# Kernel tuning notes

Measured on AMD Instinct MI355X. Metric: run time of the kernel, lower is better.

The kernel has to match this reference:

```python
import jax, jax.numpy as jnp
import numpy as np

B, A, GS = 4, 256, 12           # graphs, atoms per graph, grid size
NG = GS ** 3                    # 1728 grid nodes per graph
K_A, K_G = 8, 32                # atom kNN, grid->atom kNN
L, CODE, HID, EDGE = 4, 64, 128, 64
NTYPES, NGAUSS, CUT, SPACING = 16, 20, 5.0, 1.5
N_NODES = B * A + B * NG


def _grid_coords():
    half = (GS - 1) * SPACING / 2.0
    g = jnp.linspace(-half, half, GS)
    mesh = jnp.meshgrid(g, g, g, indexing='ij')
    return jnp.stack(mesh, axis=-1).reshape(-1, 3)  # [NG, 3]


def _gauss_consts():
    # GaussianSmearing(type_='exp', start=0, stop=cutoff, num_gaussians=20)
    off = jnp.exp(jnp.linspace(np.log(1.0), np.log(CUT + 1.0), NGAUSS)) - 1.0
    d = jnp.diff(off)
    d = jnp.concatenate([d[:1], d])
    return off, -0.5 / d ** 2


def _build_edges(pos):
    # pos: [B*A, 3] atom coords, per-graph kNN (batch = 256 atoms per graph)
    atom_pos = pos.reshape(B, A, 3)
    # atom-atom kNN (loop=False): edge (neighbor j -> atom i)
    d2 = jnp.sum((atom_pos[:, :, None, :] - atom_pos[:, None, :, :]) ** 2, -1)
    d2 = d2 + jnp.eye(A) * 1e9  # exclude self loops
    _, nbr = jax.lax.top_k(-d2, K_A)                       # [B, A, K_A]
    src_a = (nbr + (jnp.arange(B) * A)[:, None, None]).reshape(-1)
    dst_a = jnp.repeat(jnp.arange(B * A), K_A)
    # grid->atom kNN: each grid node receives from its K_G nearest atoms
    grid = _grid_coords()
    gd2 = jnp.sum((grid[None, :, None, :] - atom_pos[:, None, :, :]) ** 2, -1)  # [B, NG, A]
    _, gn = jax.lax.top_k(-gd2, K_G)                       # [B, NG, K_G]
    src_g = (gn + (jnp.arange(B) * A)[:, None, None]).reshape(-1)
    dst_g = B * A + jnp.repeat(jnp.arange(B * NG), K_G)
    return jnp.concatenate([src_a, src_g]), jnp.concatenate([dst_a, dst_g])


def _layer(h, node_pos, src, dst, cnt, off, coeff, eW, eb, W1, b1, W2, b2, g, beta):
    rel = node_pos[src] - node_pos[dst]
    dist = jnp.clip(jnp.sqrt(jnp.sum(rel ** 2, -1)), 0.0, CUT)
    gauss = jnp.exp(coeff * (dist[:, None] - off) ** 2)    # [E, 20]
    ef = gauss @ eW + eb                                   # [E, EDGE]
    mi = jnp.concatenate([h[src], h[dst], ef], -1)         # [E, 2*CODE+EDGE]
    m = jax.nn.relu(mi @ W1 + b1) @ W2 + b2                # [E, CODE]
    aggr = jax.ops.segment_sum(m, dst, num_segments=N_NODES) / cnt[:, None]
    x = h + aggr
    mu = jnp.mean(x, -1, keepdims=True)
    var = jnp.var(x, -1, keepdims=True)
    return (x - mu) / jnp.sqrt(var + 1e-5) * g + beta


def setup_inputs() -> dict:
    key = jax.random.key(0)
    ks = jax.random.split(key, 6)
    s = 0.05
    return {
        'pos': jax.random.uniform(ks[0], (B * A, 3), minval=-8.0, maxval=8.0),
        'atom_types': jax.random.randint(ks[1], (B * A,), 0, NTYPES),
        'batch': jnp.repeat(jnp.arange(B), A),
        'edge_W': jax.random.normal(ks[2], (L, NGAUSS, EDGE)) * s,
        'edge_b': jnp.zeros((L, EDGE)),
        'W1': jax.random.normal(ks[3], (L, 2 * CODE + EDGE, HID)) * s,
        'b1': jnp.zeros((L, HID)),
        'W2': jax.random.normal(ks[4], (L, HID, CODE)) * s,
        'b2': jnp.zeros((L, CODE)),
        'ln_g': jnp.ones((L, CODE)),
        'ln_b': jnp.zeros((L, CODE)),
    }


def reference(pos, atom_types, batch, edge_W, edge_b, W1, b1, W2, b2, ln_g, ln_b):
    # node features: one-hot atoms padded to code_dim, zero grid codes
    af = jax.nn.one_hot(atom_types, NTYPES, dtype=jnp.float32)
    af = jnp.pad(af, ((0, 0), (0, CODE - NTYPES)))
    h = jnp.concatenate([af, jnp.zeros((B * NG, CODE), jnp.float32)], 0)
    node_pos = jnp.concatenate([pos, jnp.tile(_grid_coords(), (B, 1))], 0)
    src, dst = _build_edges(pos)
    cnt = jnp.clip(jax.ops.segment_sum(jnp.ones_like(dst, jnp.float32), dst,
                                       num_segments=N_NODES), 1.0)
    off, coeff = _gauss_consts()
    for l in range(L):
        h = _layer(h, node_pos, src, dst, cnt, off, coeff,
                   edge_W[l], edge_b[l], W1[l], b1[l], W2[l], b2[l],
                   ln_g[l], ln_b[l])
    return h[B * A:].reshape(B, NG, CODE)
```

## Files before the change

kernel.cpp:

```cpp
#include <hip/hip_runtime.h>
#include <hip/hip_bf16.h>
#include <math.h>

#define NATOMS 1024
#define NGRID  6912
#define NNODES 7936
#define NG_PER 1728
#define KA 8
#define KG 32
#define CODE 64
#define HID 128
#define NT 1024

typedef __hip_bfloat16 bf16;
typedef unsigned long long u64;
typedef unsigned int u32;

static void* g_buf = nullptr;
__attribute__((constructor)) static void _alloc_ws(){
  if (hipMalloc(&g_buf, (size_t)24 * 1024 * 1024) != hipSuccess) g_buf = nullptr;
}

__device__ __forceinline__ float ldf(const void* p, size_t i, int f32){
  return f32 ? ((const float*)p)[i] : __bfloat162float(((const bf16*)p)[i]);
}

__device__ __forceinline__ int ldt(const void* p, int i, int mode){
  switch(mode){
    case 1:  return ((const int*)p)[2*i];
    case 2:  return (int)((const float*)p)[i];
    case 3:  return (int)__bfloat162float(((const bf16*)p)[i]);
    default: return ((const int*)p)[i];
  }
}

__global__ void k0(const unsigned short* __restrict__ posu,
                   const unsigned short* __restrict__ typu,
                   int* __restrict__ flag, float* __restrict__ offc){
  if (blockIdx.x == 0){
    __shared__ int scnt;
    int t = threadIdx.x;
    if (t == 0) scnt = 0;
    __syncthreads();
    int c = 0;
    for (int q = 0; q < 12; q++){
      unsigned short u = posu[t + 256*q];
      int e = (u >> 7) & 0xFF;
      if (e >= 140) c++;
    }
    atomicAdd(&scnt, c);
    __syncthreads();
    if (t == 0) flag[0] = (scnt > 16) ? 1 : 0;
  } else {
    if (threadIdx.x == 0){
      int oddHigh = 0, evenHigh = 0, quadZero = 1;
      for (int k = 0; k < 16; k++){
        unsigned short o = typu[2*k+1], e = typu[2*k];
        if (o >= 0x3F00 && o <= 0x4200) oddHigh++;
        if (e >= 0x3F00 && e <= 0x4200) evenHigh++;
      }
      for (int k = 0; k < 16; k++) if (typu[4*k+2] != 0) quadZero = 0;
      int mode;
      if (oddHigh >= 8) mode = (evenHigh >= 8) ? 3 : 2;
      else              mode = quadZero ? 1 : 0;
      flag[1] = mode;
    }
    int k = (int)threadIdx.x - 64;
    if (k >= 0 && k < 20){
      double step = log(6.0) / 19.0;
      double offk = exp((double)k * step) - 1.0;
      int km = (k == 0) ? 1 : k;
      double d = (exp((double)km * step) - 1.0) - (exp((double)(km - 1) * step) - 1.0);
      offc[k]      = (float)offk;
      offc[20 + k] = (float)(-0.5 / (d * d));
    }
  }
}

__global__ void __launch_bounds__(256) k_pre(const void* __restrict__ pos,
    const void* __restrict__ types, const int* __restrict__ flag,
    float* __restrict__ node_pos, float* __restrict__ h0,
    int* __restrict__ nbrA, int* __restrict__ nbrG){
  #pragma clang fp contract(off)
  int f32 = flag[0];
  int b = blockIdx.x;
  int t = threadIdx.x;
  if (b < 1984){
    int tm = flag[1];
    int idx = b * 256 + t;
    if (idx < NNODES){
      if (idx < NATOMS){
        node_pos[idx*3+0] = ldf(pos, idx*3+0, f32);
        node_pos[idx*3+1] = ldf(pos, idx*3+1, f32);
        node_pos[idx*3+2] = ldf(pos, idx*3+2, f32);
      } else {
        int cell = (idx - NATOMS) % NG_PER;
        int ix = cell / 144, iy = (cell / 12) % 12, iz = cell % 12;
        node_pos[idx*3+0] = -8.25f + 1.5f * ix;
        node_pos[idx*3+1] = -8.25f + 1.5f * iy;
        node_pos[idx*3+2] = -8.25f + 1.5f * iz;
      }
    }
    int node = idx >> 6, c = idx & 63;
    float v = 0.f;
    if (node < NATOMS && c == ldt(types, node, tm)) v = 1.f;
    h0[idx] = v;
  } else if (b < 1984 + 256){
    int i = (b - 1984) * 4 + (t >> 6);
    int bb = i >> 8, li = i & 255;
    int l = t & 63;
    float px = ldf(pos,3*i,f32), py = ldf(pos,3*i+1,f32), pz = ldf(pos,3*i+2,f32);
    u64 vals[4];
    for (int q = 0; q < 4; q++){
      int c = l + 64*q;
      int j = (bb << 8) + c;
      float dx = ldf(pos,3*j+0,f32) - px;
      float dy = ldf(pos,3*j+1,f32) - py;
      float dz = ldf(pos,3*j+2,f32) - pz;
      float d2 = (dx*dx + dy*dy) + dz*dz;
      vals[q] = (c == li) ? ~0ull : (((u64)__float_as_uint(d2) << 8) | (unsigned)c);
    }
    for (int it = 0; it < KA; it++){
      u64 v = vals[0];
      for (int q = 1; q < 4; q++) if (vals[q] < v) v = vals[q];
      for (int m = 1; m < 64; m <<= 1){
        u64 ov = __shfl_xor(v, m);
        if (ov < v) v = ov;
      }
      int widx = (int)(v & 0xFF);
      if (l == 0) nbrA[i*KA + it] = (bb << 8) + widx;
      if ((widx & 63) == l) vals[widx >> 6] = ~0ull;
    }
  } else {
    int gi = (b - 2240) * 4 + (t >> 6);
    int bb = gi / NG_PER, cell = gi % NG_PER;
    int ix = cell / 144, iy = (cell / 12) % 12, iz = cell % 12;
    double px = -8.25 + 1.5 * ix;
    double py = -8.25 + 1.5 * iy;
    double pz = -8.25 + 1.5 * iz;
    int l = t & 63;
    u64 vals[4];
    for (int q = 0; q < 4; q++){
      int c = l + 64*q;
      int j = (bb << 8) + c;
      double dx = px - (double)ldf(pos,3*j+0,f32);
      double dy = py - (double)ldf(pos,3*j+1,f32);
      double dz = pz - (double)ldf(pos,3*j+2,f32);
      double d2 = dx*dx + dy*dy + dz*dz;
      vals[q] = ((u64)__double_as_longlong(d2) & ~0xFFull) | (unsigned)c;
    }
    for (int it = 0; it < KG; it++){
      u64 v = vals[0];
      for (int q = 1; q < 4; q++) if (vals[q] < v) v = vals[q];
      for (int m = 1; m < 64; m <<= 1){
        u64 ov = __shfl_xor(v, m);
        if (ov < v) v = ov;
      }
      int widx = (int)(v & 0xFF);
      if (l == 0) nbrG[gi*KG + it] = (bb << 8) + widx;
      if ((widx & 63) == l) vals[widx >> 6] = ~0ull;
    }
  }
}

__global__ void __launch_bounds__(128) k_fold(const float* __restrict__ hin,
    const void* __restrict__ W1, const void* __restrict__ b1,
    const void* __restrict__ eW, const void* __restrict__ eb,
    size_t wl, size_t b1o, size_t eWo, size_t ebo,
    const int* __restrict__ flag,
    float* __restrict__ Xd, float* __restrict__ Xs,
    float* __restrict__ Wg, float* __restrict__ b1p,
    const float* __restrict__ offc, float* __restrict__ Tt)
{
  __shared__ __attribute__((aligned(16))) float sA[1344];
  __shared__ float sB[160];
  int f32 = flag[0];
  int t = threadIdx.x;
  int b = blockIdx.x;
  if (b < 1120){
    int isXd = (b < 992);
    size_t wo = wl + (isXd ? (size_t)64*128 : 0);
    int r0 = (isXd ? b : (b - 992)) * 8;
    float* C = isXd ? Xd : Xs;
    float w[64];
    #pragma unroll
    for (int k = 0; k < 64; k++) w[k] = ldf(W1, wo + (size_t)k*128 + t, f32);
    for (int i = t; i < 8*64; i += 128) sA[i] = hin[(size_t)r0*64 + i];
    __syncthreads();
    #pragma unroll
    for (int r = 0; r < 8; r += 4){
      float a0 = 0.f, a1 = 0.f, a2 = 0.f, a3 = 0.f;
      #pragma unroll
      for (int k4 = 0; k4 < 16; k4++){
        float4 v0 = *(const float4*)&sA[(r+0)*64 + 4*k4];
        float4 v1 = *(const float4*)&sA[(r+1)*64 + 4*k4];
        float4 v2 = *(const float4*)&sA[(r+2)*64 + 4*k4];
        float4 v3 = *(const float4*)&sA[(r+3)*64 + 4*k4];
        a0 = fmaf(v0.x, w[4*k4+0], a0); a0 = fmaf(v0.y, w[4*k4+1], a0);
        a0 = fmaf(v0.z, w[4*k4+2], a0); a0 = fmaf(v0.w, w[4*k4+3], a0);
        a1 = fmaf(v1.x, w[4*k4+0], a1); a1 = fmaf(v1.y, w[4*k4+1], a1);
        a1 = fmaf(v1.z, w[4*k4+2], a1); a1 = fmaf(v1.w, w[4*k4+3], a1);
        a2 = fmaf(v2.x, w[4*k4+0], a2); a2 = fmaf(v2.y, w[4*k4+1], a2);
        a2 = fmaf(v2.z, w[4*k4+2], a2); a2 = fmaf(v2.w, w[4*k4+3], a2);
        a3 = fmaf(v3.x, w[4*k4+0], a3); a3 = fmaf(v3.y, w[4*k4+1], a3);
        a3 = fmaf(v3.z, w[4*k4+2], a3); a3 = fmaf(v3.w, w[4*k4+3], a3);
      }
      C[(size_t)(r0 + r + 0)*128 + t] = a0;
      C[(size_t)(r0 + r + 1)*128 + t] = a1;
      C[(size_t)(r0 + r + 2)*128 + t] = a2;
      C[(size_t)(r0 + r + 3)*128 + t] = a3;
    }
  } else if (b == 1120){
    float w[64];
    #pragma unroll
    for (int k = 0; k < 64; k++) w[k] = ldf(W1, wl + (size_t)128*128 + (size_t)k*128 + t, f32);
    for (int i = t; i < 20*64; i += 128) sA[i] = ldf(eW, eWo + i, f32);
    if (t < 64) sA[1280 + t] = ldf(eb, ebo + t, f32);
    __syncthreads();
    for (int g = 0; g < 20; g++){
      float acc = 0.f;
      #pragma unroll
      for (int k4 = 0; k4 < 16; k4++){
        float4 e = *(const float4*)&sA[g*64 + 4*k4];
        acc = fmaf(e.x, w[4*k4+0], acc); acc = fmaf(e.y, w[4*k4+1], acc);
        acc = fmaf(e.z, w[4*k4+2], acc); acc = fmaf(e.w, w[4*k4+3], acc);
      }
      Wg[g*128 + t] = acc;
    }
    float acc = ldf(b1, b1o + t, f32);
    #pragma unroll
    for (int k4 = 0; k4 < 16; k4++){
      float4 e = *(const float4*)&sA[1280 + 4*k4];
      acc = fmaf(e.x, w[4*k4+0], acc); acc = fmaf(e.y, w[4*k4+1], acc);
      acc = fmaf(e.z, w[4*k4+2], acc); acc = fmaf(e.w, w[4*k4+3], acc);
    }
    b1p[t] = acc;
  } else {
    int r0 = (b - 1121) * 8;
    float w[64];
    #pragma unroll
    for (int k = 0; k < 64; k++) w[k] = ldf(W1, wl + (size_t)128*128 + (size_t)k*128 + t, f32);
    for (int i = t; i < 20*64; i += 128) sA[i] = ldf(eW, eWo + i, f32);
    for (int i = t; i < 160; i += 128){
      int row = i / 20, k = i - row*20;
      float d  = (float)(r0 + row) * (5.0f / (float)NT);
      float dd = d - offc[k];
      sB[i] = expf(offc[20 + k] * dd * dd);
    }
    __syncthreads();
    float wg[20];
    #pragma unroll
    for (int gk = 0; gk < 20; gk++){
      float acc = 0.f;
      #pragma unroll
      for (int k4 = 0; k4 < 16; k4++){
        float4 e = *(const float4*)&sA[gk*64 + 4*k4];
        acc = fmaf(e.x, w[4*k4+0], acc); acc = fmaf(e.y, w[4*k4+1], acc);
        acc = fmaf(e.z, w[4*k4+2], acc); acc = fmaf(e.w, w[4*k4+3], acc);
      }
      wg[gk] = acc;
    }
    #pragma unroll
    for (int r = 0; r < 8; r++){
      int row = r0 + r;
      if (row <= NT){
        float acc = 0.f;
        #pragma unroll
        for (int k = 0; k < 20; k++) acc = fmaf(sB[r*20 + k], wg[k], acc);
        Tt[(size_t)row*128 + t] = acc;
      }
    }
  }
}

__global__ void __launch_bounds__(256) k_aggr(const float* __restrict__ Xs,
    const float* __restrict__ Xd, const int* __restrict__ nbrA,
    const int* __restrict__ nbrG, const float* __restrict__ node_pos,
    const float* __restrict__ Tt, const float* __restrict__ b1p,
    float* __restrict__ Sbuf)
{
  __shared__ __attribute__((aligned(16))) int   sN[256];
  __shared__ __attribute__((aligned(16))) float sX[256];
  int t = threadIdx.x;
  int b = blockIdx.x;
  int KK, node0; const int* nbr;
  if (b < 32){ KK = 8;  node0 = b*32;              nbr = nbrA + b*256; }
  else       { KK = 32; node0 = NATOMS + (b-32)*8; nbr = nbrG + (size_t)(b-32)*256; }
  {
    int src = nbr[t];
    sN[t] = src;
    int node = node0 + ((b < 32) ? (t >> 3) : (t >> 5));
    float dx = node_pos[src*3+0] - node_pos[node*3+0];
    float dy = node_pos[src*3+1] - node_pos[node*3+1];
    float dz = node_pos[src*3+2] - node_pos[node*3+2];
    float dist = fminf(sqrtf(dx*dx + dy*dy + dz*dz), 5.0f);
    sX[t] = dist * ((float)NT / 5.0f);
  }
  int g = t >> 7, tt = t & 127;
  float b1v = b1p[tt];
  __syncthreads();
  float rK = 1.f / KK;
  int nLoc = (b < 32) ? 16 : 4;
  int nbase = g * nLoc;
  for (int n = 0; n < nLoc; n++){
    int node = node0 + nbase + n;
    float zb = Xd[(size_t)node*128 + tt] + b1v;
    float S = 0.f;
    int ebase = (nbase + n) * KK;
    for (int e = 0; e < KK; e += 4){
      int i0 = ebase + e;
      int4   sv = *(const int4*)&sN[i0];
      float4 xv = *(const float4*)&sX[i0];
      int ia0 = (int)xv.x; if (ia0 > NT-1) ia0 = NT-1;
      int ia1 = (int)xv.y; if (ia1 > NT-1) ia1 = NT-1;
      int ia2 = (int)xv.z; if (ia2 > NT-1) ia2 = NT-1;
      int ia3 = (int)xv.w; if (ia3 > NT-1) ia3 = NT-1;
      float f0 = xv.x - (float)ia0;
      float f1 = xv.y - (float)ia1;
      float f2 = xv.z - (float)ia2;
      float f3 = xv.w - (float)ia3;
      const float* t0 = Tt + (size_t)ia0*128 + tt;
      const float* t1 = Tt + (size_t)ia1*128 + tt;
      const float* t2 = Tt + (size_t)ia2*128 + tt;
      const float* t3 = Tt + (size_t)ia3*128 + tt;
      float v00 = t0[0], v01 = t0[128];
      float v10 = t1[0], v11 = t1[128];
      float v20 = t2[0], v21 = t2[128];
      float v30 = t3[0], v31 = t3[128];
      float a0 = zb + Xs[(size_t)sv.x*128 + tt] + fmaf(f0, v01 - v00, v00);
      float a1 = zb + Xs[(size_t)sv.y*128 + tt] + fmaf(f1, v11 - v10, v10);
      float a2 = zb + Xs[(size_t)sv.z*128 + tt] + fmaf(f2, v21 - v20, v20);
      float a3 = zb + Xs[(size_t)sv.w*128 + tt] + fmaf(f3, v31 - v30, v30);
      S += fmaxf(a0,0.f) + fmaxf(a1,0.f) + fmaxf(a2,0.f) + fmaxf(a3,0.f);
    }
    Sbuf[(size_t)node*128 + tt] = S * rK;
  }
}

__global__ void __launch_bounds__(256) k_out(const float* __restrict__ hin,
    const float* __restrict__ Sbuf,
    const void* __restrict__ W2, const void* __restrict__ b2,
    const void* __restrict__ lng, const void* __restrict__ lnb,
    size_t w2o, size_t b2o, size_t lno,
    const int* __restrict__ flag,
    float* __restrict__ hout, float* __restrict__ out, int writeOut)
{
  __shared__ float sW2[128*64];
  __shared__ __attribute__((aligned(16))) float sS[32*128];
  int f32 = flag[0];
  int t = threadIdx.x;
  int r0 = blockIdx.x * 32;
  for (int i = t; i < 128*64; i += 256) sW2[i] = ldf(W2, w2o + i, f32);
  for (int i = t; i < 32*128; i += 256) sS[i] = Sbuf[(size_t)r0*128 + i];
  int w = t >> 6, c = t & 63;
  float b2v = ldf(b2, b2o + c, f32);
  float gv  = ldf(lng, lno + c, f32);
  float bv  = ldf(lnb, lno + c, f32);
  __syncthreads();
  for (int rr = w*8; rr < w*8 + 8; rr += 2){
    float a0 = 0.f, a1 = 0.f;
    const float* s0 = &sS[rr*128];
    const float* s1 = &sS[(rr+1)*128];
    #pragma unroll
    for (int kq = 0; kq < 32; kq++){
      float4 sv0 = *(const float4*)(s0 + 4*kq);
      float4 sv1 = *(const float4*)(s1 + 4*kq);
      a0 = fmaf(sv0.x, sW2[(4*kq+0)*64+c], a0);
      a0 = fmaf(sv0.y, sW2[(4*kq+1)*64+c], a0);
      a0 = fmaf(sv0.z, sW2[(4*kq+2)*64+c], a0);
      a0 = fmaf(sv0.w, sW2[(4*kq+3)*64+c], a0);
      a1 = fmaf(sv1.x, sW2[(4*kq+0)*64+c], a1);
      a1 = fmaf(sv1.y, sW2[(4*kq+1)*64+c], a1);
      a1 = fmaf(sv1.z, sW2[(4*kq+2)*64+c], a1);
      a1 = fmaf(sv1.w, sW2[(4*kq+3)*64+c], a1);
    }
    {
      int node = r0 + rr;
      float x = hin[(size_t)node*64 + c] + a0 + b2v;
      float s = x;
      #pragma unroll
      for (int m = 1; m < 64; m <<= 1) s += __shfl_xor(s, m);
      float mu = s * (1.f/64.f);
      float d = x - mu;
      float v = d * d;
      #pragma unroll
      for (int m = 1; m < 64; m <<= 1) v += __shfl_xor(v, m);
      v *= (1.f/64.f);
      float o = d / sqrtf(v + 1e-5f) * gv + bv;
      hout[(size_t)node*64 + c] = o;
      if (writeOut && node >= NATOMS) out[(size_t)(node - NATOMS)*64 + c] = o;
    }
    {
      int node = r0 + rr + 1;
      float x = hin[(size_t)node*64 + c] + a1 + b2v;
      float s = x;
      #pragma unroll
      for (int m = 1; m < 64; m <<= 1) s += __shfl_xor(s, m);
      float mu = s * (1.f/64.f);
      float d = x - mu;
      float v = d * d;
      #pragma unroll
      for (int m = 1; m < 64; m <<= 1) v += __shfl_xor(v, m);
      v *= (1.f/64.f);
      float o = d / sqrtf(v + 1e-5f) * gv + bv;
      hout[(size_t)node*64 + c] = o;
      if (writeOut && node >= NATOMS) out[(size_t)(node - NATOMS)*64 + c] = o;
    }
  }
}

extern "C" void kernel_launch(void* const* d_in, const int* in_sizes, int n_in,
                              void* d_out, int out_size, void* d_ws, size_t ws_size,
                              hipStream_t stream) {
  const void* pos    = d_in[0];
  const void* types  = d_in[1];
  const void* edge_W = d_in[3];
  const void* edge_b = d_in[4];
  const void* W1     = d_in[5];
  const void* b1     = d_in[6];
  const void* W2     = d_in[7];
  const void* b2     = d_in[8];
  const void* lng    = d_in[9];
  const void* lnb    = d_in[10];

  const size_t NEED = (size_t)16 * 1024 * 1024;
  char* w = (ws_size >= NEED) ? (char*)d_ws : (char*)g_buf;
  if (w == nullptr) w = (char*)d_ws;

  size_t o = 0;
  auto alloc = [&](size_t bytes)->char*{
    char* r = w + o; o = (o + bytes + 255) & ~(size_t)255; return r;
  };
  float*  node_pos = (float*) alloc((size_t)NNODES*3*4);
  float*  hA       = (float*) alloc((size_t)NNODES*CODE*4);
  float*  hB       = (float*) alloc((size_t)NNODES*CODE*4);
  float*  Xs       = (float*) alloc((size_t)NATOMS*HID*4);
  float*  Xd       = (float*) alloc((size_t)NNODES*HID*4);
  float*  Sbuf     = (float*) alloc((size_t)NNODES*HID*4);
  int*    nbrA     = (int*)   alloc((size_t)NATOMS*KA*4);
  int*    nbrG     = (int*)   alloc((size_t)NGRID*KG*4);
  float*  offc     = (float*) alloc(64*4);
  float*  Wg       = (float*) alloc(20*HID*4);
  float*  b1p      = (float*) alloc(HID*4);
  int*    flag     = (int*)   alloc(64*4);
  float*  Tt       = (float*) alloc((size_t)(NT+1)*HID*4);

  k0<<<2, 256, 0, stream>>>((const unsigned short*)pos,
                            (const unsigned short*)types, flag, offc);
  k_pre<<<3968, 256, 0, stream>>>(pos, types, flag, node_pos, hA, nbrA, nbrG);

  float* hin = hA; float* hout = hB;
  for (int l = 0; l < 4; l++){
    size_t wl  = (size_t)l*192*128;
    size_t eWo = (size_t)l*20*64, ebo = (size_t)l*64;
    size_t b1o = (size_t)l*128,   w2o = (size_t)l*128*64;
    size_t b2o = (size_t)l*64,    lno = (size_t)l*64;
    k_fold<<<1121 + 129, 128, 0, stream>>>(hin, W1, b1, edge_W, edge_b,
                                     wl, b1o, eWo, ebo, flag, Xd, Xs, Wg, b1p,
                                     offc, Tt);
    k_aggr<<<32 + NGRID/8, 256, 0, stream>>>(Xs, Xd, nbrA, nbrG, node_pos,
                                             Tt, b1p, Sbuf);
    k_out<<<NNODES/32, 256, 0, stream>>>(hin, Sbuf, W2, b2, lng, lnb,
                                         w2o, b2o, lno, flag,
                                         hout, (float*)d_out, (l == 3) ? 1 : 0);
    float* tmp = hin; hin = hout; hout = tmp;
  }
}
```

Measured before the change: 359.6 us.

## Replace iterative grid kNN selection with rank counting; pack lerp table pairs

New measurement: 371.8 us. 3.4% more time.

```diff
diff --git a/kernel.cpp b/kernel.cpp
--- a/kernel.cpp
+++ b/kernel.cpp
@@ -82,6 +82,7 @@
     float* __restrict__ node_pos, float* __restrict__ h0,
     int* __restrict__ nbrA, int* __restrict__ nbrG){
   #pragma clang fp contract(off)
+  __shared__ __attribute__((aligned(16))) u64 sK[4][256];
   int f32 = flag[0];
   int b = blockIdx.x;
   int t = threadIdx.x;
@@ -132,14 +133,17 @@
       if ((widx & 63) == l) vals[widx >> 6] = ~0ull;
     }
   } else {
-    int gi = (b - 2240) * 4 + (t >> 6);
+    int w  = t >> 6;
+    int gi = (b - 2240) * 4 + w;
     int bb = gi / NG_PER, cell = gi % NG_PER;
     int ix = cell / 144, iy = (cell / 12) % 12, iz = cell % 12;
     double px = -8.25 + 1.5 * ix;
     double py = -8.25 + 1.5 * iy;
     double pz = -8.25 + 1.5 * iz;
     int l = t & 63;
+    u64* sk = &sK[w][0];
     u64 vals[4];
+    #pragma unroll
     for (int q = 0; q < 4; q++){
       int c = l + 64*q;
       int j = (bb << 8) + c;
@@ -147,19 +151,25 @@
       double dy = py - (double)ldf(pos,3*j+1,f32);
       double dz = pz - (double)ldf(pos,3*j+2,f32);
       double d2 = dx*dx + dy*dy + dz*dz;
-      vals[q] = ((u64)__double_as_longlong(d2) & ~0xFFull) | (unsigned)c;
-    }
-    for (int it = 0; it < KG; it++){
-      u64 v = vals[0];
-      for (int q = 1; q < 4; q++) if (vals[q] < v) v = vals[q];
-      for (int m = 1; m < 64; m <<= 1){
-        u64 ov = __shfl_xor(v, m);
-        if (ov < v) v = ov;
-      }
-      int widx = (int)(v & 0xFF);
-      if (l == 0) nbrG[gi*KG + it] = (bb << 8) + widx;
-      if ((widx & 63) == l) vals[widx >> 6] = ~0ull;
-    }
+      u64 key = ((u64)__double_as_longlong(d2) & ~0xFFull) | (unsigned)c;
+      vals[q] = key;
+      sk[c] = key;
+    }
+    __syncthreads();
+    int r0 = 0, r1 = 0, r2 = 0, r3 = 0;
+    #pragma unroll 4
+    for (int j = 0; j < 256; j += 2){
+      ulonglong2 kk = *(const ulonglong2*)&sk[j];
+      r0 += (kk.x < vals[0]); r0 += (kk.y < vals[0]);
+      r1 += (kk.x < vals[1]); r1 += (kk.y < vals[1]);
+      r2 += (kk.x < vals[2]); r2 += (kk.y < vals[2]);
+      r3 += (kk.x < vals[3]); r3 += (kk.y < vals[3]);
+    }
+    int base = (bb << 8) + l;
+    if (r0 < KG) nbrG[gi*KG + r0] = base;
+    if (r1 < KG) nbrG[gi*KG + r1] = base + 64;
+    if (r2 < KG) nbrG[gi*KG + r2] = base + 128;
+    if (r3 < KG) nbrG[gi*KG + r3] = base + 192;
   }
 }
 
@@ -170,10 +180,10 @@
     const int* __restrict__ flag,
     float* __restrict__ Xd, float* __restrict__ Xs,
     float* __restrict__ Wg, float* __restrict__ b1p,
-    const float* __restrict__ offc, float* __restrict__ Tt)
+    const float* __restrict__ offc, float2* __restrict__ Tt)
 {
   __shared__ __attribute__((aligned(16))) float sA[1344];
-  __shared__ float sB[160];
+  __shared__ float sB[192];
   int f32 = flag[0];
   int t = threadIdx.x;
   int b = blockIdx.x;
@@ -241,7 +251,7 @@
     #pragma unroll
     for (int k = 0; k < 64; k++) w[k] = ldf(W1, wl + (size_t)128*128 + (size_t)k*128 + t, f32);
     for (int i = t; i < 20*64; i += 128) sA[i] = ldf(eW, eWo + i, f32);
-    for (int i = t; i < 160; i += 128){
+    for (int i = t; i < 180; i += 128){
       int row = i / 20, k = i - row*20;
       float d  = (float)(r0 + row) * (5.0f / (float)NT);
       float dd = d - offc[k];
@@ -260,23 +270,24 @@
       }
       wg[gk] = acc;
     }
-    #pragma unroll
-    for (int r = 0; r < 8; r++){
-      int row = r0 + r;
-      if (row <= NT){
-        float acc = 0.f;
-        #pragma unroll
-        for (int k = 0; k < 20; k++) acc = fmaf(sB[r*20 + k], wg[k], acc);
-        Tt[(size_t)row*128 + t] = acc;
-      }
-    }
+    float v[9];
+    #pragma unroll
+    for (int r = 0; r < 9; r++){
+      float acc = 0.f;
+      #pragma unroll
+      for (int k = 0; k < 20; k++) acc = fmaf(sB[r*20 + k], wg[k], acc);
+      v[r] = acc;
+    }
+    #pragma unroll
+    for (int r = 0; r < 8; r++)
+      Tt[(size_t)(r0 + r)*128 + t] = make_float2(v[r], v[r+1]);
   }
 }
 
 __global__ void __launch_bounds__(256) k_aggr(const float* __restrict__ Xs,
     const float* __restrict__ Xd, const int* __restrict__ nbrA,
     const int* __restrict__ nbrG, const float* __restrict__ node_pos,
-    const float* __restrict__ Tt, const float* __restrict__ b1p,
+    const float2* __restrict__ Tt, const float* __restrict__ b1p,
     float* __restrict__ Sbuf)
 {
   __shared__ __attribute__((aligned(16))) int   sN[256];
@@ -319,18 +330,14 @@
       float f1 = xv.y - (float)ia1;
       float f2 = xv.z - (float)ia2;
       float f3 = xv.w - (float)ia3;
-      const float* t0 = Tt + (size_t)ia0*128 + tt;
-      const float* t1 = Tt + (size_t)ia1*128 + tt;
-      const float* t2 = Tt + (size_t)ia2*128 + tt;
-      const float* t3 = Tt + (size_t)ia3*128 + tt;
-      float v00 = t0[0], v01 = t0[128];
-      float v10 = t1[0], v11 = t1[128];
-      float v20 = t2[0], v21 = t2[128];
-      float v30 = t3[0], v31 = t3[128];
-      float a0 = zb + Xs[(size_t)sv.x*128 + tt] + fmaf(f0, v01 - v00, v00);
-      float a1 = zb + Xs[(size_t)sv.y*128 + tt] + fmaf(f1, v11 - v10, v10);
-      float a2 = zb + Xs[(size_t)sv.z*128 + tt] + fmaf(f2, v21 - v20, v20);
-      float a3 = zb + Xs[(size_t)sv.w*128 + tt] + fmaf(f3, v31 - v30, v30);
+      float2 w0 = Tt[(size_t)ia0*128 + tt];
+      float2 w1 = Tt[(size_t)ia1*128 + tt];
+      float2 w2 = Tt[(size_t)ia2*128 + tt];
+      float2 w3 = Tt[(size_t)ia3*128 + tt];
+      float a0 = zb + Xs[(size_t)sv.x*128 + tt] + fmaf(f0, w0.y - w0.x, w0.x);
+      float a1 = zb + Xs[(size_t)sv.y*128 + tt] + fmaf(f1, w1.y - w1.x, w1.x);
+      float a2 = zb + Xs[(size_t)sv.z*128 + tt] + fmaf(f2, w2.y - w2.x, w2.x);
+      float a3 = zb + Xs[(size_t)sv.w*128 + tt] + fmaf(f3, w3.y - w3.x, w3.x);
       S += fmaxf(a0,0.f) + fmaxf(a1,0.f) + fmaxf(a2,0.f) + fmaxf(a3,0.f);
     }
     Sbuf[(size_t)node*128 + tt] = S * rK;
@@ -443,7 +450,7 @@
   float*  Wg       = (float*) alloc(20*HID*4);
   float*  b1p      = (float*) alloc(HID*4);
   int*    flag     = (int*)   alloc(64*4);
-  float*  Tt       = (float*) alloc((size_t)(NT+1)*HID*4);
+  float2* Tt       = (float2*)alloc((size_t)NT*HID*8);
 
   k0<<<2, 256, 0, stream>>>((const unsigned short*)pos,
                             (const unsigned short*)types, flag, offc);
@@ -455,7 +462,7 @@
     size_t eWo = (size_t)l*20*64, ebo = (size_t)l*64;
     size_t b1o = (size_t)l*128,   w2o = (size_t)l*128*64;
     size_t b2o = (size_t)l*64,    lno = (size_t)l*64;
-    k_fold<<<1121 + 129, 128, 0, stream>>>(hin, W1, b1, edge_W, edge_b,
+    k_fold<<<1121 + 128, 128, 0, stream>>>(hin, W1, b1, edge_W, edge_b,
                                      wl, b1o, eWo, ebo, flag, Xd, Xs, Wg, b1p,
                                      offc, Tt);
     k_aggr<<<32 + NGRID/8, 256, 0, stream>>>(Xs, Xd, nbrA, nbrG, node_pos,
```
